# Optimization experiments

Hardware: AMD Instinct MI355X
Metric: run time of the kernel (lower is better)

## Reference

```python
import jax, jax.numpy as jnp
import numpy as np

RADIUS = 0.1
MAX_GRID_DIM = 96
MAX_COLLISIONS = 128


def setup_inputs() -> dict:
    key = jax.random.key(0)
    k1, k2 = jax.random.split(key)
    locs = jax.random.uniform(k1, (2, 4096, 3), dtype=jnp.float32)
    data = jax.random.normal(k2, (2, 4096, 16), dtype=jnp.float32)
    return {"locs": locs, "data": data}


def _cell_ids(locs):
    # Reproduces the grid-bound math in ParticleCollision.forward.
    lower = locs.min(axis=1)   # [B,D]
    upper = locs.max(axis=1)   # [B,D]
    grid_dims = jnp.ceil(jnp.clip((upper - lower) / RADIUS, 0.0, MAX_GRID_DIM))
    center = (lower + upper) * 0.5
    lower = center - grid_dims * RADIUS * 0.5
    gd = jnp.maximum(grid_dims, 1.0)
    cells = jnp.floor((locs - lower[:, None, :]) / RADIUS)
    cells = jnp.clip(cells, 0.0, gd[:, None, :] - 1.0).astype(jnp.int32)
    gdi = gd.astype(jnp.int32)  # [B,D]
    # Row-major strides per batch: stride[d] = prod(gdi[d+1:])
    rev_cp = jnp.cumprod(gdi[:, ::-1], axis=1)[:, ::-1]  # [B,D]
    strides = jnp.concatenate(
        [rev_cp[:, 1:], jnp.ones((gdi.shape[0], 1), jnp.int32)], axis=1)
    return (cells * strides[:, None, :]).sum(-1)  # [B,N]


def reference(locs, data):
    B, N, D = locs.shape
    cell_ids = _cell_ids(locs)
    # Stable sort by cell id (mirrors the radix sort); idxs = original index
    # of each particle in the new (sorted) order.
    order = jnp.argsort(cell_ids, axis=1, stable=True)  # [B,N]
    locs_s = jnp.take_along_axis(locs, order[:, :, None], axis=1)  # reordered locs
    data_s = jnp.take_along_axis(data, order[:, :, None], axis=1)  # reordered data
    # Pairwise squared distances without materializing [B,N,N,D].
    sq = (locs_s * locs_s).sum(-1)  # [B,N]
    d2 = sq[:, :, None] + sq[:, None, :] - 2.0 * jnp.einsum(
        'bnd,bmd->bnm', locs_s, locs_s)  # [B,N,N]
    mask = d2 <= RADIUS * RADIUS
    # First MAX_COLLISIONS in-radius neighbors per particle (ascending index
    # in sorted order), -1 padding past the end of each neighbor list.
    keys = jnp.where(mask, jnp.int32(0), jnp.int32(1))
    nbr = jnp.argsort(keys, axis=-1, stable=True)[:, :, :MAX_COLLISIONS]
    valid = jnp.take_along_axis(mask, nbr, axis=-1)
    neighbors = jnp.where(valid, nbr, -1).astype(jnp.float32)  # [B,N,M]
    idxs = order.astype(jnp.float32)  # [B,N]
    return idxs, neighbors, locs_s, data_s
```

## Files before the change

kernel.cpp:

```cpp
#include <hip/hip_runtime.h>

#define NPART 4096
#define NBATCH 2
#define MAXC 128

__global__ __launch_bounds__(256) void rank_kernel(
    const float* __restrict__ locs, unsigned short* __restrict__ partial,
    int njlog2, int jspan) {
  const int bx = blockIdx.x;
  const int tid = threadIdx.x;
  const int jslice = bx & ((1 << njlog2) - 1);
  const int ic = (bx >> njlog2) & 15;
  const int b = bx >> (njlog2 + 4);

  __shared__ float smn[3][256];
  __shared__ float smx[3][256];
  __shared__ int scj[256];
  __shared__ float sb_lower[3];
  __shared__ int sb_gdi[3];

  const float* base = locs + (size_t)b * NPART * 3;
  float mn0 = 1e30f, mn1 = 1e30f, mn2 = 1e30f;
  float mx0 = -1e30f, mx1 = -1e30f, mx2 = -1e30f;
  for (int n = tid; n < NPART; n += 256) {
    float x = base[n * 3 + 0];
    float y = base[n * 3 + 1];
    float z = base[n * 3 + 2];
    mn0 = fminf(mn0, x); mx0 = fmaxf(mx0, x);
    mn1 = fminf(mn1, y); mx1 = fmaxf(mx1, y);
    mn2 = fminf(mn2, z); mx2 = fmaxf(mx2, z);
  }
  smn[0][tid] = mn0; smn[1][tid] = mn1; smn[2][tid] = mn2;
  smx[0][tid] = mx0; smx[1][tid] = mx1; smx[2][tid] = mx2;
  __syncthreads();
  for (int s = 128; s > 0; s >>= 1) {
    if (tid < s) {
      for (int d = 0; d < 3; d++) {
        smn[d][tid] = fminf(smn[d][tid], smn[d][tid + s]);
        smx[d][tid] = fmaxf(smx[d][tid], smx[d][tid + s]);
      }
    }
    __syncthreads();
  }
  if (tid == 0) {
    for (int d = 0; d < 3; d++) {
      float lo = smn[d][0];
      float up = smx[d][0];
      float t = (up - lo) / 0.1f;
      t = fminf(fmaxf(t, 0.0f), 96.0f);
      float gdim = ceilf(t);
      float ctr = (lo + up) * 0.5f;
      float l2 = ctr - ((gdim * 0.1f) * 0.5f);
      float g = fmaxf(gdim, 1.0f);
      sb_lower[d] = l2;
      sb_gdi[d] = (int)g;
    }
  }
  __syncthreads();

  auto cid = [&](int n) {
    int c[3];
    for (int d = 0; d < 3; d++) {
      float v = base[n * 3 + d];
      float cf = floorf((v - sb_lower[d]) / 0.1f);
      float gdf = (float)sb_gdi[d];
      cf = fminf(fmaxf(cf, 0.0f), gdf - 1.0f);
      c[d] = (int)cf;
    }
    return (c[0] * sb_gdi[1] + c[1]) * sb_gdi[2] + c[2];
  };

  const int ci = cid(ic * 256 + tid);
  int cnt = 0;
  for (int jj = 0; jj < jspan; jj++) {
    int jc = jslice * jspan + jj;
    __syncthreads();
    scj[tid] = cid(jc * 256 + tid);
    __syncthreads();
    if (jc < ic) {
#pragma unroll 8
      for (int j = 0; j < 256; j++) cnt += (scj[j] <= ci);
    } else if (jc > ic) {
#pragma unroll 8
      for (int j = 0; j < 256; j++) cnt += (scj[j] < ci);
    } else {
#pragma unroll 8
      for (int j = 0; j < 256; j++) {
        int cj = scj[j];
        cnt += (cj < ci) || (cj == ci && j < tid);
      }
    }
  }
  partial[(size_t)jslice * (NBATCH * NPART) + b * NPART + ic * 256 + tid] =
      (unsigned short)cnt;
}

__global__ __launch_bounds__(256) void scatgather_kernel(
    const float* __restrict__ locs, const float* __restrict__ data,
    const unsigned short* __restrict__ partial, int nj,
    float* __restrict__ out_idxs, float* __restrict__ out_locs,
    float* __restrict__ out_data, float4* __restrict__ slocs) {
  int p = blockIdx.x * 256 + threadIdx.x;
  int pb = p >> 12;
  int i = p & (NPART - 1);
  int r = 0;
  for (int s = 0; s < nj; s++)
    r += (int)partial[(size_t)s * (NBATCH * NPART) + p];
  const float* src = locs + (size_t)p * 3;
  float x = src[0], y = src[1], z = src[2];
  float sq = __fadd_rn(__fadd_rn(__fmul_rn(x, x), __fmul_rn(y, y)),
                       __fmul_rn(z, z));
  size_t dst = (size_t)pb * NPART + r;
  out_idxs[dst] = (float)i;
  out_locs[dst * 3 + 0] = x;
  out_locs[dst * 3 + 1] = y;
  out_locs[dst * 3 + 2] = z;
  slocs[dst] = make_float4(x, y, z, sq);
  const float4* dsrc = (const float4*)(data + (size_t)p * 16);
  float4* ddst = (float4*)(out_data + dst * 16);
  for (int k = 0; k < 4; k++) ddst[k] = dsrc[k];
}

__global__ __launch_bounds__(256) void nbr_kernel(
    const float4* __restrict__ slocs, float* __restrict__ out_nbr) {
  int b = blockIdx.y;
  __shared__ float4 sl[2048];
  int wave = threadIdx.x >> 6, lane = threadIdx.x & 63;
  int row0 = blockIdx.x * 8 + wave * 2;
  const float4* sb = slocs + (size_t)b * NPART;
  float4 me0 = sb[row0 + 0];
  float4 me1 = sb[row0 + 1];
  float* r0 = out_nbr + ((size_t)b * NPART + row0) * MAXC;
  float* r1 = r0 + MAXC;
  int c0 = 0, c1 = 0;
  unsigned long long lmask = (1ull << lane) - 1ull;
  for (int half = 0; half < 2; half++) {
    int hbase = half * 2048;
    __syncthreads();
    for (int j = threadIdx.x; j < 2048; j += 256) sl[j] = sb[hbase + j];
    __syncthreads();
    for (int base = 0; base < 2048; base += 64) {
      float4 o = sl[base + lane];
      float fm = (float)(hbase + base + lane);
#define DO_ROW(ME, CN, RP)                                                  \
      {                                                                     \
        float dot = __fmaf_rn(ME.z, o.z,                                    \
                     __fmaf_rn(ME.y, o.y, __fmul_rn(ME.x, o.x)));           \
        float d2 = __fsub_rn(__fadd_rn(ME.w, o.w), __fmul_rn(2.0f, dot));   \
        bool hit = d2 <= 0.01f;                                             \
        unsigned long long bal = __ballot(hit);                             \
        int pos = CN + __popcll(bal & lmask);                               \
        if (hit && pos < MAXC) RP[pos] = fm;                                \
        CN += __popcll(bal);                                                \
      }
      DO_ROW(me0, c0, r0)
      DO_ROW(me1, c1, r1)
#undef DO_ROW
    }
  }
  for (int q = min(c0, MAXC) + lane; q < MAXC; q += 64) r0[q] = -1.0f;
  for (int q = min(c1, MAXC) + lane; q < MAXC; q += 64) r1[q] = -1.0f;
}

extern "C" void kernel_launch(void* const* d_in, const int* in_sizes, int n_in,
                              void* d_out, int out_size, void* d_ws,
                              size_t ws_size, hipStream_t stream) {
  const float* locs = (const float*)d_in[0];
  const float* data = (const float*)d_in[1];

  float* out = (float*)d_out;
  float* out_idxs = out;
  float* out_nbr = out + NBATCH * NPART;
  float* out_locs = out_nbr + (size_t)NBATCH * NPART * MAXC;
  float* out_data = out_locs + (size_t)NBATCH * NPART * 3;

  float4* slocs = (float4*)d_ws;
  unsigned short* partial =
      (unsigned short*)((char*)d_ws + (size_t)NBATCH * NPART * 16);

  size_t base_bytes = (size_t)NBATCH * NPART * 16;
  int nj, njlog2;
  if (ws_size >= base_bytes + 16ull * NBATCH * NPART * 2) {
    nj = 16; njlog2 = 4;
  } else {
    nj = 4; njlog2 = 2;
  }
  int jspan = 16 / nj;

  rank_kernel<<<NBATCH * 16 * nj, 256, 0, stream>>>(locs, partial, njlog2,
                                                    jspan);
  scatgather_kernel<<<NBATCH * NPART / 256, 256, 0, stream>>>(
      locs, data, partial, nj, out_idxs, out_locs, out_data, slocs);
  nbr_kernel<<<dim3(NPART / 8, NBATCH), 256, 0, stream>>>(slocs, out_nbr);
}
```

Baseline: 91.16 us.

## Merge rank partials in-kernel and fuse scatter with neighbor search

The rank kernel now computes every cell id into shared memory and splits each particle's full rank count across 16 lanes, reduced with shuffles, so no partial-count array or separate summation pass is needed. It writes the rank, an inverse order array, and per-particle float4 locations. A single finish kernel then does the scatter of outputs in its first 32 blocks and the neighbor search in the rest, gathering sorted locations through the order array into a 64KB shared tile and handling 4 rows per wave. This drops one launch and the slocs round trip, in exchange for each rank block recomputing all cell ids and larger shared memory reducing occupancy.

```diff
diff --git a/kernel.cpp b/kernel.cpp
--- a/kernel.cpp
+++ b/kernel.cpp
@@ -5,21 +5,21 @@
 #define MAXC 128
 
 __global__ __launch_bounds__(256) void rank_kernel(
-    const float* __restrict__ locs, unsigned short* __restrict__ partial,
-    int njlog2, int jspan) {
+    const float* __restrict__ locs, int* __restrict__ rank,
+    int* __restrict__ order, float4* __restrict__ sorig) {
   const int bx = blockIdx.x;
   const int tid = threadIdx.x;
-  const int jslice = bx & ((1 << njlog2) - 1);
-  const int ic = (bx >> njlog2) & 15;
-  const int b = bx >> (njlog2 + 4);
+  const int b = bx >> 8;
+  const int g = bx & 255;
 
   __shared__ float smn[3][256];
   __shared__ float smx[3][256];
-  __shared__ int scj[256];
+  __shared__ int scj[NPART];
   __shared__ float sb_lower[3];
   __shared__ int sb_gdi[3];
 
   const float* base = locs + (size_t)b * NPART * 3;
+
   float mn0 = 1e30f, mn1 = 1e30f, mn2 = 1e30f;
   float mx0 = -1e30f, mx1 = -1e30f, mx2 = -1e30f;
   for (int n = tid; n < NPART; n += 256) {
@@ -51,14 +51,15 @@
       float gdim = ceilf(t);
       float ctr = (lo + up) * 0.5f;
       float l2 = ctr - ((gdim * 0.1f) * 0.5f);
-      float g = fmaxf(gdim, 1.0f);
+      float g2 = fmaxf(gdim, 1.0f);
       sb_lower[d] = l2;
-      sb_gdi[d] = (int)g;
+      sb_gdi[d] = (int)g2;
     }
   }
   __syncthreads();
 
-  auto cid = [&](int n) {
+  for (int k = 0; k < 16; k++) {
+    int n = tid + k * 256;
     int c[3];
     for (int d = 0; d < 3; d++) {
       float v = base[n * 3 + d];
@@ -67,99 +68,107 @@
       cf = fminf(fmaxf(cf, 0.0f), gdf - 1.0f);
       c[d] = (int)cf;
     }
-    return (c[0] * sb_gdi[1] + c[1]) * sb_gdi[2] + c[2];
-  };
+    scj[n] = (c[0] * sb_gdi[1] + c[1]) * sb_gdi[2] + c[2];
+  }
+  __syncthreads();
 
-  const int ci = cid(ic * 256 + tid);
+  const int il = tid >> 4;
+  const int q = tid & 15;
+  const int i = g * 16 + il;
+  const int ci = scj[i];
   int cnt = 0;
-  for (int jj = 0; jj < jspan; jj++) {
-    int jc = jslice * jspan + jj;
-    __syncthreads();
-    scj[tid] = cid(jc * 256 + tid);
-    __syncthreads();
-    if (jc < ic) {
+  const int jb = q * 256;
 #pragma unroll 8
-      for (int j = 0; j < 256; j++) cnt += (scj[j] <= ci);
-    } else if (jc > ic) {
-#pragma unroll 8
-      for (int j = 0; j < 256; j++) cnt += (scj[j] < ci);
-    } else {
-#pragma unroll 8
-      for (int j = 0; j < 256; j++) {
-        int cj = scj[j];
-        cnt += (cj < ci) || (cj == ci && j < tid);
-      }
-    }
+  for (int it = 0; it < 256; it++) {
+    int j = jb + ((it + q) & 255);
+    int cj = scj[j];
+    cnt += (cj < ci) || (cj == ci && j < i);
   }
-  partial[(size_t)jslice * (NBATCH * NPART) + b * NPART + ic * 256 + tid] =
-      (unsigned short)cnt;
+  cnt += __shfl_down(cnt, 8);
+  cnt += __shfl_down(cnt, 4);
+  cnt += __shfl_down(cnt, 2);
+  cnt += __shfl_down(cnt, 1);
+  if (q == 0) {
+    int p = b * NPART + i;
+    rank[p] = cnt;
+    order[b * NPART + cnt] = i;
+    float x = base[i * 3 + 0];
+    float y = base[i * 3 + 1];
+    float z = base[i * 3 + 2];
+    float sq = __fadd_rn(__fadd_rn(__fmul_rn(x, x), __fmul_rn(y, y)),
+                         __fmul_rn(z, z));
+    sorig[p] = make_float4(x, y, z, sq);
+  }
 }
 
-__global__ __launch_bounds__(256) void scatgather_kernel(
+__global__ __launch_bounds__(256) void finish_kernel(
     const float* __restrict__ locs, const float* __restrict__ data,
-    const unsigned short* __restrict__ partial, int nj,
-    float* __restrict__ out_idxs, float* __restrict__ out_locs,
-    float* __restrict__ out_data, float4* __restrict__ slocs) {
-  int p = blockIdx.x * 256 + threadIdx.x;
-  int pb = p >> 12;
-  int i = p & (NPART - 1);
-  int r = 0;
-  for (int s = 0; s < nj; s++)
-    r += (int)partial[(size_t)s * (NBATCH * NPART) + p];
-  const float* src = locs + (size_t)p * 3;
-  float x = src[0], y = src[1], z = src[2];
-  float sq = __fadd_rn(__fadd_rn(__fmul_rn(x, x), __fmul_rn(y, y)),
-                       __fmul_rn(z, z));
-  size_t dst = (size_t)pb * NPART + r;
-  out_idxs[dst] = (float)i;
-  out_locs[dst * 3 + 0] = x;
-  out_locs[dst * 3 + 1] = y;
-  out_locs[dst * 3 + 2] = z;
-  slocs[dst] = make_float4(x, y, z, sq);
-  const float4* dsrc = (const float4*)(data + (size_t)p * 16);
-  float4* ddst = (float4*)(out_data + dst * 16);
-  for (int k = 0; k < 4; k++) ddst[k] = dsrc[k];
-}
-
-__global__ __launch_bounds__(256) void nbr_kernel(
-    const float4* __restrict__ slocs, float* __restrict__ out_nbr) {
-  int b = blockIdx.y;
-  __shared__ float4 sl[2048];
-  int wave = threadIdx.x >> 6, lane = threadIdx.x & 63;
-  int row0 = blockIdx.x * 8 + wave * 2;
-  const float4* sb = slocs + (size_t)b * NPART;
-  float4 me0 = sb[row0 + 0];
-  float4 me1 = sb[row0 + 1];
+    const int* __restrict__ rank, const int* __restrict__ order,
+    const float4* __restrict__ sorig, float* __restrict__ out_idxs,
+    float* __restrict__ out_nbr, float* __restrict__ out_locs,
+    float* __restrict__ out_data) {
+  const int bx = blockIdx.x;
+  if (bx < 32) {
+    int p = bx * 256 + threadIdx.x;
+    int pb = p >> 12;
+    int i = p & (NPART - 1);
+    int r = rank[p];
+    const float* src = locs + (size_t)p * 3;
+    float x = src[0], y = src[1], z = src[2];
+    size_t dst = (size_t)pb * NPART + r;
+    out_idxs[dst] = (float)i;
+    out_locs[dst * 3 + 0] = x;
+    out_locs[dst * 3 + 1] = y;
+    out_locs[dst * 3 + 2] = z;
+    const float4* dsrc = (const float4*)(data + (size_t)p * 16);
+    float4* ddst = (float4*)(out_data + dst * 16);
+    for (int k = 0; k < 4; k++) ddst[k] = dsrc[k];
+    return;
+  }
+  __shared__ float4 sl[NPART];
+  const int kb = bx - 32;
+  const int b = kb >> 8;
+  const int g = kb & 255;
+  const int* ob = order + b * NPART;
+  const float4* sb = sorig + (size_t)b * NPART;
+  for (int j = threadIdx.x; j < NPART; j += 256) sl[j] = sb[ob[j]];
+  __syncthreads();
+  const int wave = threadIdx.x >> 6, lane = threadIdx.x & 63;
+  const int row0 = g * 16 + wave * 4;
+  float4 me0 = sl[row0 + 0];
+  float4 me1 = sl[row0 + 1];
+  float4 me2 = sl[row0 + 2];
+  float4 me3 = sl[row0 + 3];
   float* r0 = out_nbr + ((size_t)b * NPART + row0) * MAXC;
   float* r1 = r0 + MAXC;
-  int c0 = 0, c1 = 0;
-  unsigned long long lmask = (1ull << lane) - 1ull;
-  for (int half = 0; half < 2; half++) {
-    int hbase = half * 2048;
-    __syncthreads();
-    for (int j = threadIdx.x; j < 2048; j += 256) sl[j] = sb[hbase + j];
-    __syncthreads();
-    for (int base = 0; base < 2048; base += 64) {
-      float4 o = sl[base + lane];
-      float fm = (float)(hbase + base + lane);
+  float* r2 = r1 + MAXC;
+  float* r3 = r2 + MAXC;
+  int c0 = 0, c1 = 0, c2 = 0, c3 = 0;
+  const unsigned long long lmask = (1ull << lane) - 1ull;
+  for (int base = 0; base < NPART; base += 64) {
+    float4 o = sl[base + lane];
+    float fm = (float)(base + lane);
 #define DO_ROW(ME, CN, RP)                                                  \
-      {                                                                     \
-        float dot = __fmaf_rn(ME.z, o.z,                                    \
-                     __fmaf_rn(ME.y, o.y, __fmul_rn(ME.x, o.x)));           \
-        float d2 = __fsub_rn(__fadd_rn(ME.w, o.w), __fmul_rn(2.0f, dot));   \
-        bool hit = d2 <= 0.01f;                                             \
-        unsigned long long bal = __ballot(hit);                             \
-        int pos = CN + __popcll(bal & lmask);                               \
-        if (hit && pos < MAXC) RP[pos] = fm;                                \
-        CN += __popcll(bal);                                                \
-      }
-      DO_ROW(me0, c0, r0)
-      DO_ROW(me1, c1, r1)
+    {                                                                       \
+      float dot = __fmaf_rn(ME.z, o.z,                                     \
+                   __fmaf_rn(ME.y, o.y, __fmul_rn(ME.x, o.x)));            \
+      float d2 = __fsub_rn(__fadd_rn(ME.w, o.w), __fmul_rn(2.0f, dot));    \
+      bool hit = d2 <= 0.01f;                                              \
+      unsigned long long bal = __ballot(hit);                              \
+      int pos = CN + __popcll(bal & lmask);                                \
+      if (hit && pos < MAXC) RP[pos] = fm;                                 \
+      CN += __popcll(bal);                                                 \
+    }
+    DO_ROW(me0, c0, r0)
+    DO_ROW(me1, c1, r1)
+    DO_ROW(me2, c2, r2)
+    DO_ROW(me3, c3, r3)
 #undef DO_ROW
-    }
   }
-  for (int q = min(c0, MAXC) + lane; q < MAXC; q += 64) r0[q] = -1.0f;
-  for (int q = min(c1, MAXC) + lane; q < MAXC; q += 64) r1[q] = -1.0f;
+  for (int p2 = min(c0, MAXC) + lane; p2 < MAXC; p2 += 64) r0[p2] = -1.0f;
+  for (int p2 = min(c1, MAXC) + lane; p2 < MAXC; p2 += 64) r1[p2] = -1.0f;
+  for (int p2 = min(c2, MAXC) + lane; p2 < MAXC; p2 += 64) r2[p2] = -1.0f;
+  for (int p2 = min(c3, MAXC) + lane; p2 < MAXC; p2 += 64) r3[p2] = -1.0f;
 }
 
 extern "C" void kernel_launch(void* const* d_in, const int* in_sizes, int n_in,
@@ -174,22 +183,12 @@
   float* out_locs = out_nbr + (size_t)NBATCH * NPART * MAXC;
   float* out_data = out_locs + (size_t)NBATCH * NPART * 3;
 
-  float4* slocs = (float4*)d_ws;
-  unsigned short* partial =
-      (unsigned short*)((char*)d_ws + (size_t)NBATCH * NPART * 16);
+  float4* sorig = (float4*)d_ws;
+  int* order = (int*)((char*)d_ws + (size_t)NBATCH * NPART * 16);
+  int* rank = (int*)((char*)d_ws + (size_t)NBATCH * NPART * 16 +
+                     (size_t)NBATCH * NPART * 4);
 
-  size_t base_bytes = (size_t)NBATCH * NPART * 16;
-  int nj, njlog2;
-  if (ws_size >= base_bytes + 16ull * NBATCH * NPART * 2) {
-    nj = 16; njlog2 = 4;
-  } else {
-    nj = 4; njlog2 = 2;
-  }
-  int jspan = 16 / nj;
-
-  rank_kernel<<<NBATCH * 16 * nj, 256, 0, stream>>>(locs, partial, njlog2,
-                                                    jspan);
-  scatgather_kernel<<<NBATCH * NPART / 256, 256, 0, stream>>>(
-      locs, data, partial, nj, out_idxs, out_locs, out_data, slocs);
-  nbr_kernel<<<dim3(NPART / 8, NBATCH), 256, 0, stream>>>(slocs, out_nbr);
+  rank_kernel<<<NBATCH * 256, 256, 0, stream>>>(locs, rank, order, sorig);
+  finish_kernel<<<32 + NBATCH * 256, 256, 0, stream>>>(
+      locs, data, rank, order, sorig, out_idxs, out_nbr, out_locs, out_data);
 }
```

Result: slower. 117.3 us (+28.6%).

## Cull neighbor chunks by bounding boxes and process four rows per wave

Applied to the files above, without the earlier changes.

In the neighbor kernel, a per-64-particle bounding box is computed for each chunk of sorted particles in shared memory. A wave skips a chunk entirely when the chunk's box lies farther than the radius (with a small margin) from the box around the wave's own rows. Each wave now handles four rows instead of two, which halves the grid. Because particles are sorted by cell, chunks are spatially compact and many distance tests can be culled. The cost is the extra shuffle reductions, an extra barrier and fewer blocks in flight.

```diff
diff --git a/kernel.cpp b/kernel.cpp
--- a/kernel.cpp
+++ b/kernel.cpp
@@ -123,25 +123,59 @@
 
 __global__ __launch_bounds__(256) void nbr_kernel(
     const float4* __restrict__ slocs, float* __restrict__ out_nbr) {
-  int b = blockIdx.y;
+  const int b = blockIdx.y;
   __shared__ float4 sl[2048];
-  int wave = threadIdx.x >> 6, lane = threadIdx.x & 63;
-  int row0 = blockIdx.x * 8 + wave * 2;
+  __shared__ float cbb[32][6];
+  const int tid = threadIdx.x;
+  const int wave = tid >> 6, lane = tid & 63;
+  const int row0 = blockIdx.x * 16 + wave * 4;
   const float4* sb = slocs + (size_t)b * NPART;
   float4 me0 = sb[row0 + 0];
   float4 me1 = sb[row0 + 1];
+  float4 me2 = sb[row0 + 2];
+  float4 me3 = sb[row0 + 3];
+  float wlx = fminf(fminf(me0.x, me1.x), fminf(me2.x, me3.x));
+  float whx = fmaxf(fmaxf(me0.x, me1.x), fmaxf(me2.x, me3.x));
+  float wly = fminf(fminf(me0.y, me1.y), fminf(me2.y, me3.y));
+  float why = fmaxf(fmaxf(me0.y, me1.y), fmaxf(me2.y, me3.y));
+  float wlz = fminf(fminf(me0.z, me1.z), fminf(me2.z, me3.z));
+  float whz = fmaxf(fmaxf(me0.z, me1.z), fmaxf(me2.z, me3.z));
   float* r0 = out_nbr + ((size_t)b * NPART + row0) * MAXC;
   float* r1 = r0 + MAXC;
-  int c0 = 0, c1 = 0;
-  unsigned long long lmask = (1ull << lane) - 1ull;
+  float* r2 = r1 + MAXC;
+  float* r3 = r2 + MAXC;
+  int c0 = 0, c1 = 0, c2 = 0, c3 = 0;
+  const unsigned long long lmask = (1ull << lane) - 1ull;
   for (int half = 0; half < 2; half++) {
-    int hbase = half * 2048;
-    __syncthreads();
-    for (int j = threadIdx.x; j < 2048; j += 256) sl[j] = sb[hbase + j];
-    __syncthreads();
-    for (int base = 0; base < 2048; base += 64) {
-      float4 o = sl[base + lane];
-      float fm = (float)(hbase + base + lane);
+    const int hbase = half * 2048;
+    __syncthreads();
+    for (int j = tid; j < 2048; j += 256) sl[j] = sb[hbase + j];
+    __syncthreads();
+    for (int c = wave; c < 32; c += 4) {
+      float4 v = sl[c * 64 + lane];
+      float lx = v.x, hx = v.x, ly = v.y, hy = v.y, lz = v.z, hz = v.z;
+      for (int s = 32; s > 0; s >>= 1) {
+        lx = fminf(lx, __shfl_xor(lx, s));
+        hx = fmaxf(hx, __shfl_xor(hx, s));
+        ly = fminf(ly, __shfl_xor(ly, s));
+        hy = fmaxf(hy, __shfl_xor(hy, s));
+        lz = fminf(lz, __shfl_xor(lz, s));
+        hz = fmaxf(hz, __shfl_xor(hz, s));
+      }
+      if (lane == 0) {
+        cbb[c][0] = lx; cbb[c][1] = hx;
+        cbb[c][2] = ly; cbb[c][3] = hy;
+        cbb[c][4] = lz; cbb[c][5] = hz;
+      }
+    }
+    __syncthreads();
+    for (int c = 0; c < 32; c++) {
+      float dx = fmaxf(fmaxf(cbb[c][0] - whx, wlx - cbb[c][1]), 0.0f);
+      float dy = fmaxf(fmaxf(cbb[c][2] - why, wly - cbb[c][3]), 0.0f);
+      float dz = fmaxf(fmaxf(cbb[c][4] - whz, wlz - cbb[c][5]), 0.0f);
+      if (dx * dx + dy * dy + dz * dz > 0.0102f) continue;
+      float4 o = sl[c * 64 + lane];
+      float fm = (float)(hbase + c * 64 + lane);
 #define DO_ROW(ME, CN, RP)                                                  \
       {                                                                     \
         float dot = __fmaf_rn(ME.z, o.z,                                    \
@@ -155,11 +189,15 @@
       }
       DO_ROW(me0, c0, r0)
       DO_ROW(me1, c1, r1)
+      DO_ROW(me2, c2, r2)
+      DO_ROW(me3, c3, r3)
 #undef DO_ROW
     }
   }
   for (int q = min(c0, MAXC) + lane; q < MAXC; q += 64) r0[q] = -1.0f;
   for (int q = min(c1, MAXC) + lane; q < MAXC; q += 64) r1[q] = -1.0f;
+  for (int q = min(c2, MAXC) + lane; q < MAXC; q += 64) r2[q] = -1.0f;
+  for (int q = min(c3, MAXC) + lane; q < MAXC; q += 64) r3[q] = -1.0f;
 }
 
 extern "C" void kernel_launch(void* const* d_in, const int* in_sizes, int n_in,
@@ -191,5 +229,5 @@
                                                     jspan);
   scatgather_kernel<<<NBATCH * NPART / 256, 256, 0, stream>>>(
       locs, data, partial, nj, out_idxs, out_locs, out_data, slocs);
-  nbr_kernel<<<dim3(NPART / 8, NBATCH), 256, 0, stream>>>(slocs, out_nbr);
-}
+  nbr_kernel<<<dim3(NPART / 16, NBATCH), 256, 0, stream>>>(slocs, out_nbr);
+}
```

Result: slower. 105.8 us (+16.0%).
